# Kernel tuning notes

Hardware: AMD Instinct MI355X
Metric: run time of the kernel (lower is better)

The kernel has to match this reference:

```python
import jax, jax.numpy as jnp
import numpy as np

HIDDEN = 2048
N_HEADS = 16
N_KV = 8
HEAD_DIM = 128
EPS = 1e-6
THETA = 1000000.0
T = 2048


def _rmsnorm(x, w):
    # x: [T, h, D]; normalize over last dim
    var = jnp.mean(x * x, axis=-1, keepdims=True)
    return x * jax.lax.rsqrt(var + EPS) * w


def _rope(x, positions):
    # neox-style rotate-half, rotary_dim == head_dim
    D = x.shape[-1]
    inv_freq = 1.0 / (THETA ** (jnp.arange(0, D, 2, dtype=jnp.float32) / D))  # [D/2]
    freqs = positions.astype(jnp.float32)[:, None] * inv_freq  # [T, D/2]
    cos = jnp.cos(freqs)[:, None, :]  # [T, 1, D/2]
    sin = jnp.sin(freqs)[:, None, :]
    x1, x2 = jnp.split(x, 2, axis=-1)
    return jnp.concatenate([x1 * cos - x2 * sin, x2 * cos + x1 * sin], axis=-1)


def setup_inputs() -> dict:
    key = jax.random.key(0)
    ks = jax.random.split(key, 7)
    s = 0.02
    return {
        "positions": jnp.arange(T, dtype=jnp.int32),
        "hidden_states": jax.random.normal(ks[0], (T, HIDDEN), dtype=jnp.float32),
        "wq": jax.random.normal(ks[1], (HIDDEN, N_HEADS * HEAD_DIM), dtype=jnp.float32) * s,
        "wk": jax.random.normal(ks[2], (HIDDEN, N_KV * HEAD_DIM), dtype=jnp.float32) * s,
        "wv": jax.random.normal(ks[3], (HIDDEN, N_KV * HEAD_DIM), dtype=jnp.float32) * s,
        "wo": jax.random.normal(ks[4], (N_HEADS * HEAD_DIM, HIDDEN), dtype=jnp.float32) * s,
        "q_norm_w": jnp.ones((HEAD_DIM,), dtype=jnp.float32),
        "k_norm_w": jnp.ones((HEAD_DIM,), dtype=jnp.float32),
    }


def reference(positions, hidden_states, wq, wk, wv, wo, q_norm_w, k_norm_w):
    q = (hidden_states @ wq).reshape(-1, N_HEADS, HEAD_DIM)
    k = (hidden_states @ wk).reshape(-1, N_KV, HEAD_DIM)
    v = (hidden_states @ wv).reshape(-1, N_KV, HEAD_DIM)
    q = _rmsnorm(q, q_norm_w)
    k = _rmsnorm(k, k_norm_w)
    q = _rope(q, positions)
    k = _rope(k, positions)
    # GQA: expand kv heads
    rep = N_HEADS // N_KV
    k = jnp.repeat(k, rep, axis=1)  # [T, H, D]
    v = jnp.repeat(v, rep, axis=1)
    scale = HEAD_DIM ** -0.5
    scores = jnp.einsum('qhd,khd->hqk', q, k) * scale  # [H, T, T]
    tq = q.shape[0]
    causal = jnp.tril(jnp.ones((tq, tq), dtype=bool))
    scores = jnp.where(causal[None], scores, jnp.finfo(scores.dtype).min)
    probs = jax.nn.softmax(scores, axis=-1)
    o = jnp.einsum('hqk,khd->qhd', probs, v).reshape(tq, N_HEADS * HEAD_DIM)
    return o @ wo
```

## Files before the change

kernel.cpp:

```cpp
#include <hip/hip_runtime.h>
#include <cstdint>

#define TT 2048
#define NH 16
#define NKV 8
#define HD 128
#define SCALE_L2E 0.12751743f
#define SM_M2 16.5f

typedef unsigned short u16;
typedef unsigned int u32;
typedef u16 u16x8 __attribute__((ext_vector_type(8)));
typedef u32 u32x2 __attribute__((ext_vector_type(2)));
typedef __bf16 bf16x8 __attribute__((ext_vector_type(8)));
typedef float f32x4 __attribute__((ext_vector_type(4)));
typedef float f32x16 __attribute__((ext_vector_type(16)));

__device__ inline u16 f2bf(float x){
  u32 u = __builtin_bit_cast(u32, x);
  u = (u + 0x7fffu + ((u >> 16) & 1u)) >> 16;
  return (u16)u;
}
__device__ inline float bf2f(u16 h){
  return __builtin_bit_cast(float, (u32)h << 16);
}
__device__ inline bf16x8 as_bf(u16x8 v){ return __builtin_bit_cast(bf16x8, v); }

__device__ inline void gl_lds16(const void* g, void* l){
  typedef __attribute__((address_space(1))) const void gv_t;
  typedef __attribute__((address_space(3))) void lv_t;
  __builtin_amdgcn_global_load_lds((gv_t*)g, (lv_t*)l, 16, 0, 0);
}

__global__ void cast_f32_bf16(const float* __restrict__ in, u16* __restrict__ out, int n8){
  int i = blockIdx.x * blockDim.x + threadIdx.x;
  if (i < n8){
    const float4* p = (const float4*)(in + (size_t)i * 8);
    float4 a = p[0], b = p[1];
    u16x8 o = { f2bf(a.x), f2bf(a.y), f2bf(a.z), f2bf(a.w),
                f2bf(b.x), f2bf(b.y), f2bf(b.z), f2bf(b.w) };
    *(u16x8*)(out + (size_t)i * 8) = o;
  }
}

__global__ void transpose_cast(const float* __restrict__ in, u16* __restrict__ out, int R, int C){
  __shared__ float tile[64][65];
  int bx = blockIdx.x * 64;
  int by = blockIdx.y * 64;
  int tid = threadIdx.x;
  #pragma unroll
  for (int i = 0; i < 4; ++i){
    int idx = i * 256 + tid;
    int r = idx >> 4, c4 = (idx & 15) * 4;
    float4 v = *(const float4*)&in[(size_t)(by + r) * C + bx + c4];
    tile[r][c4] = v.x; tile[r][c4 + 1] = v.y; tile[r][c4 + 2] = v.z; tile[r][c4 + 3] = v.w;
  }
  __syncthreads();
  #pragma unroll
  for (int i = 0; i < 2; ++i){
    int idx = i * 256 + tid;
    int cc = idx >> 3, s8 = (idx & 7) * 8;
    u16x8 o;
    #pragma unroll
    for (int j = 0; j < 8; ++j) o[j] = f2bf(tile[s8 + j][cc]);
    *(u16x8*)&out[(size_t)(bx + cc) * R + by + s8] = o;
  }
}

#define MF16(mmp, af, bf)                                                            \
  do {                                                                               \
    __builtin_amdgcn_s_setprio(1);                                                   \
    _Pragma("unroll") for (int m2 = 0; m2 < 2; m2++)                                 \
    _Pragma("unroll") for (int nn = 0; nn < 4; nn++)                                 \
    _Pragma("unroll") for (int kk = 0; kk < 2; kk++)                                 \
      acc[(mmp)*2 + m2][nn] = __builtin_amdgcn_mfma_f32_16x16x32_bf16(               \
        (af)[m2*2 + kk], (bf)[nn*2 + kk], acc[(mmp)*2 + m2][nn], 0, 0, 0);           \
    __builtin_amdgcn_s_setprio(0);                                                   \
  } while (0)

template<bool F32OUT>
__global__ __launch_bounds__(512, 2) void gemm8ph(const u16* __restrict__ A, const u16* __restrict__ B,
                                                  void* __restrict__ Cv, int Klen,
                                                  int lda, int ldb, int ldc, size_t zstride){
  extern __shared__ u16 smem[];
  const int tid = threadIdx.x;
  const int wv = tid >> 6, ln = tid & 63;
  const int lg = ln >> 4, l15 = ln & 15;
  const int wr = wv >> 2, wc = wv & 3;
  const int nbx = gridDim.x;
  const int orig = blockIdx.x + nbx * blockIdx.y;
  const int cpx = (nbx * gridDim.y) >> 3;
  const int swz = (orig & 7) * cpx + (orig >> 3);
  const int m0 = (swz / nbx) * 128, n0 = (swz % nbx) * 256;
  const int Kofs = blockIdx.z * Klen;
  const u16* Ab0 = A + (size_t)m0 * lda + Kofs;
  const u16* Bb0 = B + (size_t)n0 * ldb + Kofs;
  f32x4 acc[4][4] = {};

  auto stageA = [&](int buf, int kt, int c){
    int idx = c * 512 + tid;
    int r = idx >> 3, sl = idx & 7, g = sl ^ (r & 7);
    gl_lds16(Ab0 + (size_t)kt * 64 + (size_t)r * lda + g * 8,
             smem + buf * 24576 + (c * 512 + wv * 64) * 8);
  };
  auto stageB = [&](int buf, int kt, int q){
    int idx = q * 512 + tid;
    int r = idx >> 3, sl = idx & 7, g = sl ^ (r & 7);
    gl_lds16(Bb0 + (size_t)kt * 64 + (size_t)r * ldb + g * 8,
             smem + buf * 24576 + 8192 + (q * 512 + wv * 64) * 8);
  };
  auto ldA = [&](const u16* bufA, int mmp, bf16x8* af){
    #pragma unroll
    for (int m2 = 0; m2 < 2; m2++)
      #pragma unroll
      for (int kk = 0; kk < 2; kk++){
        int ra = wr * 64 + (mmp * 2 + m2) * 16 + l15;
        int sl = (kk * 4 + lg) ^ (ra & 7);
        af[m2 * 2 + kk] = as_bf(*(const u16x8*)&bufA[(ra * 8 + sl) * 8]);
      }
  };
  auto ldB = [&](const u16* bufB, bf16x8* bf){
    #pragma unroll
    for (int nn = 0; nn < 4; nn++)
      #pragma unroll
      for (int kk = 0; kk < 2; kk++){
        int cb = wc * 64 + nn * 16 + l15;
        int sl = (kk * 4 + lg) ^ (cb & 7);
        bf[nn * 2 + kk] = as_bf(*(const u16x8*)&bufB[(cb * 8 + sl) * 8]);
      }
  };

  const int nk = Klen / 64;
  #pragma unroll
  for (int c = 0; c < 2; ++c) stageA(0, 0, c);
  #pragma unroll
  for (int q = 0; q < 4; ++q) stageB(0, 0, q);
  #pragma unroll
  for (int c = 0; c < 2; ++c) stageA(1, 1, c);
  #pragma unroll
  for (int q = 0; q < 4; ++q) stageB(1, 1, q);
  asm volatile("s_waitcnt vmcnt(6)" ::: "memory");
  asm volatile("s_barrier" ::: "memory");

  bf16x8 af[4], bf[8];
  for (int u = 0; u < nk; u += 2){
    const int b0 = u % 3, b1 = (u + 1) % 3, b2 = (u + 2) % 3;
    const u16* A0 = smem + b0 * 24576;  const u16* B0 = A0 + 8192;
    const u16* A1 = smem + b1 * 24576;  const u16* B1 = A1 + 8192;
    const bool st = (u + 2 < nk);
    ldA(A0, 0, af); ldB(B0, bf);
    if (st){ stageA(b2, u + 2, 0); stageA(b2, u + 2, 1); stageB(b2, u + 2, 0); }
    asm volatile("s_barrier" ::: "memory");
    asm volatile("s_waitcnt lgkmcnt(0)" ::: "memory");
    __builtin_amdgcn_sched_barrier(0);
    MF16(0, af, bf);
    asm volatile("s_barrier" ::: "memory");
    ldA(A0, 1, af);
    if (st){ stageB(b2, u + 2, 1); stageB(b2, u + 2, 2); stageB(b2, u + 2, 3); }
    if (st) asm volatile("s_waitcnt vmcnt(6)" ::: "memory");
    else    asm volatile("s_waitcnt vmcnt(0)" ::: "memory");
    asm volatile("s_barrier" ::: "memory");
    asm volatile("s_waitcnt lgkmcnt(0)" ::: "memory");
    __builtin_amdgcn_sched_barrier(0);
    MF16(1, af, bf);
    asm volatile("s_barrier" ::: "memory");
    ldA(A1, 0, af); ldB(B1, bf);
    if (st){ stageA(b0, u + 3, 0); stageA(b0, u + 3, 1); stageB(b0, u + 3, 0); }
    asm volatile("s_barrier" ::: "memory");
    asm volatile("s_waitcnt lgkmcnt(0)" ::: "memory");
    __builtin_amdgcn_sched_barrier(0);
    MF16(0, af, bf);
    asm volatile("s_barrier" ::: "memory");
    ldA(A1, 1, af);
    if (st){ stageB(b0, u + 3, 1); stageB(b0, u + 3, 2); stageB(b0, u + 3, 3); }
    if (st) asm volatile("s_waitcnt vmcnt(6)" ::: "memory");
    asm volatile("s_barrier" ::: "memory");
    asm volatile("s_waitcnt lgkmcnt(0)" ::: "memory");
    __builtin_amdgcn_sched_barrier(0);
    MF16(1, af, bf);
    asm volatile("s_barrier" ::: "memory");
  }
  #pragma unroll
  for (int mm = 0; mm < 4; mm++)
    #pragma unroll
    for (int nn = 0; nn < 4; nn++){
      int grow0 = m0 + wr * 64 + mm * 16 + lg * 4;
      int gcol  = n0 + wc * 64 + nn * 16 + l15;
      #pragma unroll
      for (int r = 0; r < 4; r++){
        float v = acc[mm][nn][r];
        if (F32OUT) ((float*)Cv + blockIdx.z * zstride)[(size_t)(grow0 + r) * ldc + gcol] = v;
        else        ((u16*)Cv)[(size_t)(grow0 + r) * ldc + gcol] = f2bf(v);
      }
    }
}

__global__ __launch_bounds__(512, 2) void gemm_n128(const u16* __restrict__ A, const u16* __restrict__ B,
                                                    float* __restrict__ C, int Klen,
                                                    int lda, int ldb, int ldc){
  extern __shared__ u16 smem[];
  const int tid = threadIdx.x;
  const int wv = tid >> 6, ln = tid & 63;
  const int lg = ln >> 4, l15 = ln & 15;
  const int wr = wv >> 2, wc = wv & 3;
  const int nbx = gridDim.x;
  const int orig = blockIdx.x + nbx * blockIdx.y;
  const int cpx = (nbx * gridDim.y) >> 3;
  const int swz = (orig & 7) * cpx + (orig >> 3);
  const int m0 = (swz / nbx) * 128, n0 = (swz % nbx) * 128;
  const u16* Ab0 = A + (size_t)m0 * lda;
  const u16* Bb0 = B + (size_t)n0 * ldb;
  f32x4 acc[4][2] = {};

  auto stage4 = [&](int buf, int kt){
    #pragma unroll
    for (int c = 0; c < 2; ++c){
      int idx = c * 512 + tid;
      int r = idx >> 3, sl = idx & 7, g = sl ^ (r & 7);
      gl_lds16(Ab0 + (size_t)kt * 64 + (size_t)r * lda + g * 8,
               smem + buf * 16384 + (c * 512 + wv * 64) * 8);
    }
    #pragma unroll
    for (int q = 0; q < 2; ++q){
      int idx = q * 512 + tid;
      int r = idx >> 3, sl = idx & 7, g = sl ^ (r & 7);
      gl_lds16(Bb0 + (size_t)kt * 64 + (size_t)r * ldb + g * 8,
               smem + buf * 16384 + 8192 + (q * 512 + wv * 64) * 8);
    }
  };

  const int nk = Klen / 64;
  stage4(0, 0);
  stage4(1, 1);
  asm volatile("s_waitcnt vmcnt(4)" ::: "memory");
  asm volatile("s_barrier" ::: "memory");

  for (int u = 0; u < nk; ++u){
    const u16* A0 = smem + (u % 3) * 16384;
    const u16* B0 = A0 + 8192;
    const bool st = (u + 2 < nk);
    bf16x8 af[8], bf[4];
    #pragma unroll
    for (int mm = 0; mm < 4; mm++)
      #pragma unroll
      for (int kk = 0; kk < 2; kk++){
        int ra = wr * 64 + mm * 16 + l15;
        int sl = (kk * 4 + lg) ^ (ra & 7);
        af[mm * 2 + kk] = as_bf(*(const u16x8*)&A0[(ra * 8 + sl) * 8]);
      }
    #pragma unroll
    for (int nn = 0; nn < 2; nn++)
      #pragma unroll
      for (int kk = 0; kk < 2; kk++){
        int cb = wc * 32 + nn * 16 + l15;
        int sl = (kk * 4 + lg) ^ (cb & 7);
        bf[nn * 2 + kk] = as_bf(*(const u16x8*)&B0[(cb * 8 + sl) * 8]);
      }
    if (st) stage4((u + 2) % 3, u + 2);
    if (st) asm volatile("s_waitcnt vmcnt(4)" ::: "memory");
    else    asm volatile("s_waitcnt vmcnt(0)" ::: "memory");
    asm volatile("s_barrier" ::: "memory");
    asm volatile("s_waitcnt lgkmcnt(0)" ::: "memory");
    __builtin_amdgcn_sched_barrier(0);
    __builtin_amdgcn_s_setprio(1);
    #pragma unroll
    for (int mm = 0; mm < 4; mm++)
      #pragma unroll
      for (int nn = 0; nn < 2; nn++)
        #pragma unroll
        for (int kk = 0; kk < 2; kk++)
          acc[mm][nn] = __builtin_amdgcn_mfma_f32_16x16x32_bf16(
            af[mm * 2 + kk], bf[nn * 2 + kk], acc[mm][nn], 0, 0, 0);
    __builtin_amdgcn_s_setprio(0);
    asm volatile("s_barrier" ::: "memory");
  }
  #pragma unroll
  for (int mm = 0; mm < 4; mm++)
    #pragma unroll
    for (int nn = 0; nn < 2; nn++){
      int grow0 = m0 + wr * 64 + mm * 16 + lg * 4;
      int gcol  = n0 + wc * 32 + nn * 16 + l15;
      #pragma unroll
      for (int r = 0; r < 4; r++)
        C[(size_t)(grow0 + r) * ldc + gcol] = acc[mm][nn][r];
    }
}

__global__ void rmsnorm_rope(const u16* __restrict__ QKV, const int* __restrict__ pos,
                             const float* __restrict__ qw, const float* __restrict__ kw,
                             u16* __restrict__ Qr, u16* __restrict__ Kr){
  int gw = (blockIdx.x * blockDim.x + threadIdx.x) >> 6;
  int ln = threadIdx.x & 63;
  int t = gw / 24, idx = gw % 24;
  if (t >= TT) return;
  bool isq = idx < NH;
  int head = isq ? idx : idx - NH;
  const u16* src = QKV + (size_t)t * 4096 + (isq ? head * HD : 2048 + head * HD);
  const float* wgt = isq ? qw : kw;
  float x0 = bf2f(src[ln]), x1 = bf2f(src[ln + 64]);
  float ss = x0 * x0 + x1 * x1;
  #pragma unroll
  for (int off = 32; off; off >>= 1) ss += __shfl_xor(ss, off);
  float r = rsqrtf(ss * (1.0f / 128.0f) + 1e-6f);
  float xn0 = x0 * r * wgt[ln], xn1 = x1 * r * wgt[ln + 64];
  float inv = exp2f(-(float)ln * 0.311430758895690f);
  float ang = (float)pos[t] * inv;
  float c = cosf(ang), s = sinf(ang);
  float o0 = xn0 * c - xn1 * s;
  float o1 = xn1 * c + xn0 * s;
  u16* dst = isq ? (Qr + (size_t)t * 2048 + head * HD) : (Kr + (size_t)t * 1024 + head * HD);
  dst[ln]      = f2bf(o0);
  dst[ln + 64] = f2bf(o1);
}

__global__ void v_transpose(const u16* __restrict__ QKV, u16* __restrict__ Vt){
  __shared__ u16 tile[64][72];
  int kh = blockIdx.z;
  int d0 = blockIdx.y * 64;
  int t0 = blockIdx.x * 64;
  int tid = threadIdx.x;
  #pragma unroll
  for (int it = 0; it < 2; ++it){
    int idx = it * 256 + tid;
    int tr = idx >> 3, seg = idx & 7;
    *(u16x8*)&tile[tr][seg * 8] =
      *(const u16x8*)(QKV + (size_t)(t0 + tr) * 4096 + 3072 + kh * HD + d0 + seg * 8);
  }
  __syncthreads();
  #pragma unroll
  for (int it = 0; it < 2; ++it){
    int idx = it * 256 + tid;
    int dr = idx >> 3, seg = idx & 7;
    u16x8 v;
    #pragma unroll
    for (int j = 0; j < 8; j++) v[j] = tile[seg * 8 + j][dr];
    *(u16x8*)(Vt + ((size_t)kh * HD + d0 + dr) * 2048 + t0 + seg * 8) = v;
  }
}

__global__ __launch_bounds__(512, 4) void attn(const u16* __restrict__ Qr, const u16* __restrict__ Kr,
                                               const u16* __restrict__ Vt, u16* __restrict__ O){
  extern __shared__ u16 smem[];
  u16* Karea = smem;
  u16* Varea = smem + 16384;
  u16* Parea = smem + 32768;
  const int h = blockIdx.y, kh = h >> 1;
  const int qc = (h < 8) ? blockIdx.x : 31 - blockIdx.x;
  const int tid = threadIdx.x, wv = tid >> 6, ln = tid & 63;
  const bool isS = wv < 4;
  const int role = wv & 3;
  const int qw = role & 1, jp = role >> 1;
  const int q5 = ln & 31, hb = ln >> 5;
  const int nit = qc + 1;
  const int xr = (q5 & 3) << 1;

  auto stage = [&](int i){
    if (i + 1 < nit){
      u16* Kd = Karea + ((i + 1) & 1) * 8192;
      #pragma unroll
      for (int j = 0; j < 2; ++j){
        int lin = j * 512 + tid;
        int tok = lin >> 4, seg = lin & 15;
        gl_lds16(Kr + (size_t)((i + 1) * 64 + tok) * 1024 + kh * HD + (seg ^ (tok & 7)) * 8,
                 Kd + (j * 512 + wv * 64) * 8);
      }
    }
    if (i < nit){
      u16* Vd = Varea + (i & 1) * 8192;
      #pragma unroll
      for (int j = 0; j < 2; ++j){
        int lin = j * 512 + tid;
        int d = lin >> 3, sl = lin & 7;
        gl_lds16(Vt + (size_t)kh * HD * 2048 + (size_t)d * 2048 + i * 64 + (sl ^ (d & 7)) * 8,
                 Vd + (j * 512 + wv * 64) * 8);
      }
    }
  };

  #pragma unroll
  for (int j = 0; j < 2; ++j){
    int lin = j * 512 + tid;
    int tok = lin >> 4, seg = lin & 15;
    gl_lds16(Kr + (size_t)tok * 1024 + kh * HD + (seg ^ (tok & 7)) * 8,
             Karea + (j * 512 + wv * 64) * 8);
  }

  const u16x8 ones_u = {0x3f80, 0x3f80, 0x3f80, 0x3f80, 0x3f80, 0x3f80, 0x3f80, 0x3f80};
  const bf16x8 onesf = as_bf(ones_u);

  if (isS){
    bf16x8 qf[8];
    {
      const u16* qp = Qr + (size_t)(qc * 64 + qw * 32 + q5) * 2048 + h * HD + hb * 8;
      #pragma unroll
      for (int s = 0; s < 8; ++s) qf[s] = as_bf(*(const u16x8*)(qp + s * 16));
    }
    for (int i = 0; i <= nit; ++i){
      __syncthreads();
      stage(i);
      const int t = 2 * i + jp;
      const int D0 = 32 * t - 64 * qc - 32 * qw;
      const bool act = (i < nit) && (D0 <= 0);
      if (act){
        const u16* Kb = Karea + (i & 1) * 8192;
        const int tokIdx = 32 * jp + q5;
        f32x16 ca = {}, cb = {};
        __builtin_amdgcn_s_setprio(1);
        #pragma unroll
        for (int s = 0; s < 4; ++s){
          int seg = (2 * s + hb) ^ (q5 & 7);
          bf16x8 kf = as_bf(*(const u16x8*)&Kb[tokIdx * 128 + seg * 8]);
          ca = __builtin_amdgcn_mfma_f32_32x32x16_bf16(kf, qf[s], ca, 0, 0, 0);
        }
        #pragma unroll
        for (int s = 4; s < 8; ++s){
          int seg = (2 * s + hb) ^ (q5 & 7);
          bf16x8 kf = as_bf(*(const u16x8*)&Kb[tokIdx * 128 + seg * 8]);
          cb = __builtin_amdgcn_mfma_f32_32x32x16_bf16(kf, qf[s], cb, 0, 0, 0);
        }
        __builtin_amdgcn_s_setprio(0);
        f32x16 c = ca + cb;
        const bool diag = (D0 == 0);
        u32 pk[8];
        #pragma unroll
        for (int j = 0; j < 8; ++j){
          float pv[2];
          #pragma unroll
          for (int e = 0; e < 2; ++e){
            int r = 2 * j + e;
            int tok = (r & 3) + 8 * (r >> 2) + 4 * hb;
            float x = c[r] * SCALE_L2E - SM_M2;
            if (diag && tok > q5) x = -1e30f;
            pv[e] = exp2f(x);
          }
          pk[j] = (__builtin_bit_cast(u32, pv[0]) >> 16) |
                  (__builtin_bit_cast(u32, pv[1]) & 0xffff0000u);
        }
        u16* Pq = Parea + (i & 1) * 4096 + role * 1024 + q5 * 32;
        *(u32x2*)&Pq[((hb + 0) ^ xr) * 4] = u32x2{pk[0], pk[1]};
        *(u32x2*)&Pq[((hb + 2) ^ xr) * 4] = u32x2{pk[2], pk[3]};
        *(u32x2*)&Pq[((hb + 4) ^ xr) * 4] = u32x2{pk[4], pk[5]};
        *(u32x2*)&Pq[((hb + 6) ^ xr) * 4] = u32x2{pk[6], pk[7]};
      }
    }
    __syncthreads();
    __syncthreads();
  } else {
    f32x16 acc[4] = {};
    f32x16 asum = {};
    for (int i = 0; i <= nit; ++i){
      __syncthreads();
      stage(i);
      const int t = 2 * (i - 1) + jp;
      const int D0 = 32 * t - 64 * qc - 32 * qw;
      const bool act = (i >= 1) && (D0 <= 0);
      if (act){
        const u16* Pq = Parea + ((i - 1) & 1) * 4096 + role * 1024 + q5 * 32;
        bf16x8 pf0 = as_bf(*(const u16x8*)&Pq[((2 * hb + 0) ^ xr) * 4]);
        bf16x8 pf1 = as_bf(*(const u16x8*)&Pq[((2 * hb + 4) ^ xr) * 4]);
        const u16* Vb = Varea + ((i - 1) & 1) * 8192;
        __builtin_amdgcn_s_setprio(1);
        asum = __builtin_amdgcn_mfma_f32_32x32x16_bf16(pf0, onesf, asum, 0, 0, 0);
        asum = __builtin_amdgcn_mfma_f32_32x32x16_bf16(pf1, onesf, asum, 0, 0, 0);
        #pragma unroll
        for (int dblk = 0; dblk < 4; ++dblk){
          int d = dblk * 32 + q5;
          bf16x8 v0 = as_bf(*(const u16x8*)&Vb[d * 64 + ((4 * jp + 0 + hb) ^ (d & 7)) * 8]);
          bf16x8 v1 = as_bf(*(const u16x8*)&Vb[d * 64 + ((4 * jp + 2 + hb) ^ (d & 7)) * 8]);
          acc[dblk] = __builtin_amdgcn_mfma_f32_32x32x16_bf16(pf0, v0, acc[dblk], 0, 0, 0);
          acc[dblk] = __builtin_amdgcn_mfma_f32_32x32x16_bf16(pf1, v1, acc[dblk], 0, 0, 0);
        }
        __builtin_amdgcn_s_setprio(0);
      }
    }
    __syncthreads();
    float* Ls  = (float*)smem;
    float* LsS = (float*)smem + 8192;
    if (jp == 1){
      #pragma unroll
      for (int dblk = 0; dblk < 4; ++dblk)
        #pragma unroll
        for (int r = 0; r < 16; ++r){
          int qrow = (r & 3) + 8 * (r >> 2) + 4 * hb;
          Ls[qw * 4096 + qrow * 128 + dblk * 32 + q5] = acc[dblk][r];
        }
      if (q5 == 0){
        #pragma unroll
        for (int r = 0; r < 16; ++r){
          int qrow = (r & 3) + 8 * (r >> 2) + 4 * hb;
          LsS[qw * 32 + qrow] = asum[r];
        }
      }
    }
    __syncthreads();
    if (jp == 0){
      #pragma unroll
      for (int r = 0; r < 16; ++r){
        int qrow = (r & 3) + 8 * (r >> 2) + 4 * hb;
        float rs = 1.0f / (asum[r] + LsS[qw * 32 + qrow]);
        int qg = qc * 64 + qw * 32 + qrow;
        #pragma unroll
        for (int dblk = 0; dblk < 4; ++dblk){
          float o = (acc[dblk][r] + Ls[qw * 4096 + qrow * 128 + dblk * 32 + q5]) * rs;
          O[(size_t)qg * 2048 + h * HD + dblk * 32 + q5] = f2bf(o);
        }
      }
    }
  }
}

extern "C" void kernel_launch(void* const* d_in, const int* in_sizes, int n_in,
                              void* d_out, int out_size, void* d_ws, size_t ws_size,
                              hipStream_t stream){
  const int*   positions = (const int*)d_in[0];
  const float* hidden    = (const float*)d_in[1];
  const float* wq        = (const float*)d_in[2];
  const float* wk        = (const float*)d_in[3];
  const float* wv        = (const float*)d_in[4];
  const float* wo        = (const float*)d_in[5];
  const float* qw        = (const float*)d_in[6];
  const float* kw        = (const float*)d_in[7];
  float* out = (float*)d_out;

  char* ws = (char*)d_ws;
  u16* hs   = (u16*)ws; ws += (size_t)2048 * 2048 * 2;
  u16* Wqkv = (u16*)ws; ws += (size_t)4096 * 2048 * 2;
  u16* Wo   = (u16*)ws; ws += (size_t)2048 * 2048 * 2;
  u16* QKV  = (u16*)ws; ws += (size_t)2048 * 4096 * 2;
  u16* Qr   = (u16*)ws; ws += (size_t)2048 * 2048 * 2;
  u16* Kr   = (u16*)ws; ws += (size_t)2048 * 1024 * 2;
  u16* Vt   = (u16*)ws; ws += (size_t)8 * 128 * 2048 * 2;
  u16* O    = (u16*)ws;

  cast_f32_bf16<<<2048, 256, 0, stream>>>(hidden, hs, 2048 * 2048 / 8);
  transpose_cast<<<dim3(32, 32), 256, 0, stream>>>(wq, Wqkv, 2048, 2048);
  transpose_cast<<<dim3(16, 32), 256, 0, stream>>>(wk, Wqkv + (size_t)2048 * 2048, 2048, 1024);
  transpose_cast<<<dim3(16, 32), 256, 0, stream>>>(wv, Wqkv + (size_t)3072 * 2048, 2048, 1024);
  transpose_cast<<<dim3(32, 32), 256, 0, stream>>>(wo, Wo, 2048, 2048);

  gemm8ph<false><<<dim3(16, 16, 1), 512, 147456, stream>>>(hs, Wqkv, QKV, 2048, 2048, 2048, 4096, 0);

  rmsnorm_rope<<<2048 * 24 / 4, 256, 0, stream>>>(QKV, positions, qw, kw, Qr, Kr);
  v_transpose<<<dim3(32, 2, 8), 256, 0, stream>>>(QKV, Vt);

  attn<<<dim3(32, 16), 512, 81920, stream>>>(Qr, Kr, Vt, O);

  gemm_n128<<<dim3(16, 16), 512, 98304, stream>>>(O, Wo, out, 2048, 2048, 2048, 2048);
}
```

Measured before the change: 146.4 us.

## Double attention query tile to 128 rows per block and restructure S/PV warp roles

```diff
diff --git a/kernel.cpp b/kernel.cpp
--- a/kernel.cpp
+++ b/kernel.cpp
@@ -345,13 +345,12 @@
   u16* Varea = smem + 16384;
   u16* Parea = smem + 32768;
   const int h = blockIdx.y, kh = h >> 1;
-  const int qc = (h < 8) ? blockIdx.x : 31 - blockIdx.x;
+  const int qc = (h < 8) ? blockIdx.x : 15 - blockIdx.x;
   const int tid = threadIdx.x, wv = tid >> 6, ln = tid & 63;
   const bool isS = wv < 4;
   const int role = wv & 3;
-  const int qw = role & 1, jp = role >> 1;
   const int q5 = ln & 31, hb = ln >> 5;
-  const int nit = qc + 1;
+  const int nit = 2 * qc + 2;
   const int xr = (q5 & 3) << 1;
 
   auto stage = [&](int i){
@@ -385,125 +384,164 @@
              Karea + (j * 512 + wv * 64) * 8);
   }
 
-  const u16x8 ones_u = {0x3f80, 0x3f80, 0x3f80, 0x3f80, 0x3f80, 0x3f80, 0x3f80, 0x3f80};
-  const bf16x8 onesf = as_bf(ones_u);
-
   if (isS){
-    bf16x8 qf[8];
+    const int qs = role & 1, jp = role >> 1;
+    bf16x8 qf0[8], qf1[8];
     {
-      const u16* qp = Qr + (size_t)(qc * 64 + qw * 32 + q5) * 2048 + h * HD + hb * 8;
-      #pragma unroll
-      for (int s = 0; s < 8; ++s) qf[s] = as_bf(*(const u16x8*)(qp + s * 16));
-    }
+      const u16* qp0 = Qr + (size_t)(qc * 128 + qs * 64 + q5) * 2048 + h * HD + hb * 8;
+      const u16* qp1 = qp0 + (size_t)32 * 2048;
+      #pragma unroll
+      for (int s = 0; s < 8; ++s){ qf0[s] = as_bf(*(const u16x8*)(qp0 + s * 16));
+                                   qf1[s] = as_bf(*(const u16x8*)(qp1 + s * 16)); }
+    }
+    float asum0 = 0.f, asum1 = 0.f;
+    const int qbase0 = qc * 128 + qs * 64;
     for (int i = 0; i <= nit; ++i){
       __syncthreads();
       stage(i);
-      const int t = 2 * i + jp;
-      const int D0 = 32 * t - 64 * qc - 32 * qw;
-      const bool act = (i < nit) && (D0 <= 0);
+      const int tb = i * 64 + 32 * jp;
+      const int D1 = tb - (qbase0 + 32);
+      const int D0 = D1 + 32;
+      const bool act = (i < nit) && (D1 <= 0);
+      f32x16 c0 = {}, c1 = {};
       if (act){
         const u16* Kb = Karea + (i & 1) * 8192;
         const int tokIdx = 32 * jp + q5;
-        f32x16 ca = {}, cb = {};
         __builtin_amdgcn_s_setprio(1);
         #pragma unroll
-        for (int s = 0; s < 4; ++s){
+        for (int s = 0; s < 8; ++s){
           int seg = (2 * s + hb) ^ (q5 & 7);
           bf16x8 kf = as_bf(*(const u16x8*)&Kb[tokIdx * 128 + seg * 8]);
-          ca = __builtin_amdgcn_mfma_f32_32x32x16_bf16(kf, qf[s], ca, 0, 0, 0);
-        }
-        #pragma unroll
-        for (int s = 4; s < 8; ++s){
-          int seg = (2 * s + hb) ^ (q5 & 7);
-          bf16x8 kf = as_bf(*(const u16x8*)&Kb[tokIdx * 128 + seg * 8]);
-          cb = __builtin_amdgcn_mfma_f32_32x32x16_bf16(kf, qf[s], cb, 0, 0, 0);
+          c0 = __builtin_amdgcn_mfma_f32_32x32x16_bf16(kf, qf0[s], c0, 0, 0, 0);
+          c1 = __builtin_amdgcn_mfma_f32_32x32x16_bf16(kf, qf1[s], c1, 0, 0, 0);
         }
         __builtin_amdgcn_s_setprio(0);
-        f32x16 c = ca + cb;
-        const bool diag = (D0 == 0);
-        u32 pk[8];
-        #pragma unroll
-        for (int j = 0; j < 8; ++j){
-          float pv[2];
+      }
+      asm volatile("s_barrier" ::: "memory");
+      if (i < nit){
+        if (D1 <= 0){
+          const bool diag = (D1 == 0);
+          u32 pk[8]; float sum = 0.f;
           #pragma unroll
-          for (int e = 0; e < 2; ++e){
-            int r = 2 * j + e;
-            int tok = (r & 3) + 8 * (r >> 2) + 4 * hb;
-            float x = c[r] * SCALE_L2E - SM_M2;
-            if (diag && tok > q5) x = -1e30f;
-            pv[e] = exp2f(x);
+          for (int j = 0; j < 8; ++j){
+            float pv[2];
+            #pragma unroll
+            for (int e = 0; e < 2; ++e){
+              int r = 2 * j + e;
+              int tl = (r & 3) + 8 * (r >> 2) + 4 * hb;
+              float x = c1[r] * SCALE_L2E - SM_M2;
+              if (diag && tl > q5) x = -1e30f;
+              pv[e] = exp2f(x);
+            }
+            sum += pv[0] + pv[1];
+            pk[j] = (__builtin_bit_cast(u32, pv[0]) >> 16) |
+                    (__builtin_bit_cast(u32, pv[1]) & 0xffff0000u);
           }
-          pk[j] = (__builtin_bit_cast(u32, pv[0]) >> 16) |
-                  (__builtin_bit_cast(u32, pv[1]) & 0xffff0000u);
+          asum1 += sum;
+          u16* Pq = Parea + (2 * qs + 1) * 2048 + q5 * 64 + jp * 32;
+          #pragma unroll
+          for (int m = 0; m < 4; ++m)
+            *(u32x2*)&Pq[((hb + 2 * m) ^ xr) * 4] = u32x2{pk[2 * m], pk[2 * m + 1]};
+        } else if (jp == 1 && D1 == 32){
+          u16* Pq = Parea + (2 * qs + 1) * 2048 + q5 * 64 + jp * 32;
+          #pragma unroll
+          for (int m = 0; m < 4; ++m)
+            *(u32x2*)&Pq[((hb + 2 * m) ^ xr) * 4] = u32x2{0u, 0u};
         }
-        u16* Pq = Parea + (i & 1) * 4096 + role * 1024 + q5 * 32;
-        *(u32x2*)&Pq[((hb + 0) ^ xr) * 4] = u32x2{pk[0], pk[1]};
-        *(u32x2*)&Pq[((hb + 2) ^ xr) * 4] = u32x2{pk[2], pk[3]};
-        *(u32x2*)&Pq[((hb + 4) ^ xr) * 4] = u32x2{pk[4], pk[5]};
-        *(u32x2*)&Pq[((hb + 6) ^ xr) * 4] = u32x2{pk[6], pk[7]};
-      }
-    }
-    __syncthreads();
+        if (D0 <= 0){
+          const bool diag = (D0 == 0);
+          u32 pk[8]; float sum = 0.f;
+          #pragma unroll
+          for (int j = 0; j < 8; ++j){
+            float pv[2];
+            #pragma unroll
+            for (int e = 0; e < 2; ++e){
+              int r = 2 * j + e;
+              int tl = (r & 3) + 8 * (r >> 2) + 4 * hb;
+              float x = c0[r] * SCALE_L2E - SM_M2;
+              if (diag && tl > q5) x = -1e30f;
+              pv[e] = exp2f(x);
+            }
+            sum += pv[0] + pv[1];
+            pk[j] = (__builtin_bit_cast(u32, pv[0]) >> 16) |
+                    (__builtin_bit_cast(u32, pv[1]) & 0xffff0000u);
+          }
+          asum0 += sum;
+          u16* Pq = Parea + (2 * qs) * 2048 + q5 * 64 + jp * 32;
+          #pragma unroll
+          for (int m = 0; m < 4; ++m)
+            *(u32x2*)&Pq[((hb + 2 * m) ^ xr) * 4] = u32x2{pk[2 * m], pk[2 * m + 1]};
+        } else if (jp == 1 && D0 == 32){
+          u16* Pq = Parea + (2 * qs) * 2048 + q5 * 64 + jp * 32;
+          #pragma unroll
+          for (int m = 0; m < 4; ++m)
+            *(u32x2*)&Pq[((hb + 2 * m) ^ xr) * 4] = u32x2{0u, 0u};
+        }
+      }
+    }
+    float* asumL = (float*)smem;
+    asumL[(2 * qs + 0) * 128 + q5 * 4 + jp * 2 + hb] = asum0;
+    asumL[(2 * qs + 1) * 128 + q5 * 4 + jp * 2 + hb] = asum1;
     __syncthreads();
   } else {
-    f32x16 acc[4] = {};
-    f32x16 asum = {};
+    const int qw2 = role & 1, dp = role >> 1;
+    f32x16 acc00 = {}, acc01 = {}, acc10 = {}, acc11 = {};
+    const int qbase0 = qc * 128 + qw2 * 64;
     for (int i = 0; i <= nit; ++i){
       __syncthreads();
       stage(i);
-      const int t = 2 * (i - 1) + jp;
-      const int D0 = 32 * t - 64 * qc - 32 * qw;
-      const bool act = (i >= 1) && (D0 <= 0);
-      if (act){
-        const u16* Pq = Parea + ((i - 1) & 1) * 4096 + role * 1024 + q5 * 32;
-        bf16x8 pf0 = as_bf(*(const u16x8*)&Pq[((2 * hb + 0) ^ xr) * 4]);
-        bf16x8 pf1 = as_bf(*(const u16x8*)&Pq[((2 * hb + 4) ^ xr) * 4]);
+      const int tb = (i - 1) * 64;
+      const int D1 = tb - (qbase0 + 32);
+      const int D0 = D1 + 32;
+      const bool v1 = (i >= 1) && (D1 <= 0);
+      const bool v0 = (i >= 1) && (D0 <= 0);
+      bf16x8 pf1[4], pf0[4];
+      if (v1){
+        const u16* P1 = Parea + (2 * qw2 + 1) * 2048 + q5 * 64;
+        const u16* P0 = Parea + (2 * qw2) * 2048 + q5 * 64;
+        #pragma unroll
+        for (int ks = 0; ks < 4; ++ks){
+          int slot = 8 * (ks >> 1) + ((4 * (ks & 1) + 2 * hb) ^ xr);
+          pf1[ks] = as_bf(*(const u16x8*)&P1[slot * 4]);
+          if (v0) pf0[ks] = as_bf(*(const u16x8*)&P0[slot * 4]);
+        }
+        asm volatile("s_waitcnt lgkmcnt(0)" ::: "memory");
+        __builtin_amdgcn_sched_barrier(0);
+      }
+      asm volatile("s_barrier" ::: "memory");
+      if (v1){
         const u16* Vb = Varea + ((i - 1) & 1) * 8192;
         __builtin_amdgcn_s_setprio(1);
-        asum = __builtin_amdgcn_mfma_f32_32x32x16_bf16(pf0, onesf, asum, 0, 0, 0);
-        asum = __builtin_amdgcn_mfma_f32_32x32x16_bf16(pf1, onesf, asum, 0, 0, 0);
         #pragma unroll
-        for (int dblk = 0; dblk < 4; ++dblk){
-          int d = dblk * 32 + q5;
-          bf16x8 v0 = as_bf(*(const u16x8*)&Vb[d * 64 + ((4 * jp + 0 + hb) ^ (d & 7)) * 8]);
-          bf16x8 v1 = as_bf(*(const u16x8*)&Vb[d * 64 + ((4 * jp + 2 + hb) ^ (d & 7)) * 8]);
-          acc[dblk] = __builtin_amdgcn_mfma_f32_32x32x16_bf16(pf0, v0, acc[dblk], 0, 0, 0);
-          acc[dblk] = __builtin_amdgcn_mfma_f32_32x32x16_bf16(pf1, v1, acc[dblk], 0, 0, 0);
+        for (int ks = 0; ks < 4; ++ks){
+          int d0v = dp * 64 + q5;
+          int d1v = dp * 64 + 32 + q5;
+          bf16x8 vf0 = as_bf(*(const u16x8*)&Vb[d0v * 64 + ((2 * ks + hb) ^ (d0v & 7)) * 8]);
+          bf16x8 vf1 = as_bf(*(const u16x8*)&Vb[d1v * 64 + ((2 * ks + hb) ^ (d1v & 7)) * 8]);
+          acc10 = __builtin_amdgcn_mfma_f32_32x32x16_bf16(pf1[ks], vf0, acc10, 0, 0, 0);
+          acc11 = __builtin_amdgcn_mfma_f32_32x32x16_bf16(pf1[ks], vf1, acc11, 0, 0, 0);
+          if (v0){
+            acc00 = __builtin_amdgcn_mfma_f32_32x32x16_bf16(pf0[ks], vf0, acc00, 0, 0, 0);
+            acc01 = __builtin_amdgcn_mfma_f32_32x32x16_bf16(pf0[ks], vf1, acc01, 0, 0, 0);
+          }
         }
         __builtin_amdgcn_s_setprio(0);
       }
     }
     __syncthreads();
-    float* Ls  = (float*)smem;
-    float* LsS = (float*)smem + 8192;
-    if (jp == 1){
-      #pragma unroll
-      for (int dblk = 0; dblk < 4; ++dblk)
-        #pragma unroll
-        for (int r = 0; r < 16; ++r){
-          int qrow = (r & 3) + 8 * (r >> 2) + 4 * hb;
-          Ls[qw * 4096 + qrow * 128 + dblk * 32 + q5] = acc[dblk][r];
-        }
-      if (q5 == 0){
-        #pragma unroll
-        for (int r = 0; r < 16; ++r){
-          int qrow = (r & 3) + 8 * (r >> 2) + 4 * hb;
-          LsS[qw * 32 + qrow] = asum[r];
-        }
-      }
-    }
-    __syncthreads();
-    if (jp == 0){
+    const float* asumL = (const float*)smem;
+    #pragma unroll
+    for (int b = 0; b < 2; ++b){
       #pragma unroll
       for (int r = 0; r < 16; ++r){
         int qrow = (r & 3) + 8 * (r >> 2) + 4 * hb;
-        float rs = 1.0f / (asum[r] + LsS[qw * 32 + qrow]);
-        int qg = qc * 64 + qw * 32 + qrow;
-        #pragma unroll
-        for (int dblk = 0; dblk < 4; ++dblk){
-          float o = (acc[dblk][r] + Ls[qw * 4096 + qrow * 128 + dblk * 32 + q5]) * rs;
-          O[(size_t)qg * 2048 + h * HD + dblk * 32 + q5] = f2bf(o);
-        }
+        f32x4 s4 = *(const f32x4*)&asumL[(2 * qw2 + b) * 128 + qrow * 4];
+        float rinv = 1.0f / (s4.x + s4.y + s4.z + s4.w);
+        int qg = qc * 128 + qw2 * 64 + b * 32 + qrow;
+        float o0v = (b ? acc10[r] : acc00[r]) * rinv;
+        float o1v = (b ? acc11[r] : acc01[r]) * rinv;
+        O[(size_t)qg * 2048 + h * HD + dp * 64 + q5]      = f2bf(o0v);
+        O[(size_t)qg * 2048 + h * HD + dp * 64 + 32 + q5] = f2bf(o1v);
       }
     }
   }
@@ -543,7 +581,7 @@
   rmsnorm_rope<<<2048 * 24 / 4, 256, 0, stream>>>(QKV, positions, qw, kw, Qr, Kr);
   v_transpose<<<dim3(32, 2, 8), 256, 0, stream>>>(QKV, Vt);
 
-  attn<<<dim3(32, 16), 512, 81920, stream>>>(Qr, Kr, Vt, O);
+  attn<<<dim3(16, 16), 512, 81920, stream>>>(Qr, Kr, Vt, O);
 
   gemm_n128<<<dim3(16, 16), 512, 98304, stream>>>(O, Wo, out, 2048, 2048, 2048, 2048);
 }
```

Measured after the change: 178.6 us. 22.0% more time.
